# Performance work log

Measured on AMD Instinct MI355X. Metric: run time of the kernel, lower is better.

## Reference

```python
import jax, jax.numpy as jnp
import numpy as np

N_NODES = 100000
N_EDGES = 1600000
NUM_FEATURES = 128
HIDDEN = 64
NUM_CLASSES = 2


def _gcn_norm(edge_index, num_nodes):
    # PyG gcn_norm: add self-loops, symmetric degree normalization.
    loop = jnp.arange(num_nodes, dtype=edge_index.dtype)
    src = jnp.concatenate([edge_index[0], loop])
    dst = jnp.concatenate([edge_index[1], loop])
    deg = jax.ops.segment_sum(jnp.ones_like(src, dtype=jnp.float32), dst,
                              num_segments=num_nodes)
    dinv = jnp.where(deg > 0, jax.lax.rsqrt(deg), 0.0)
    norm = dinv[src] * dinv[dst]  # [E + N]
    return src, dst, norm


def _gcn_conv(x, src, dst, norm, W, b, num_nodes):
    h = x @ W  # linear transform first (PyG GCNConv)
    msg = h[src] * norm[:, None]  # gather + edge scaling, [E+N, H]
    out = jax.ops.segment_sum(msg, dst, num_segments=num_nodes)  # scatter-add
    return out + b


def setup_inputs() -> dict:
    key = jax.random.key(0)
    ks = jax.random.split(key, 8)
    x = jax.random.normal(ks[0], (N_NODES, NUM_FEATURES), dtype=jnp.float32)
    edge_index = jax.random.randint(ks[1], (2, N_EDGES), 0, N_NODES, dtype=jnp.int32)
    def glorot(k, shape):
        lim = np.sqrt(6.0 / (shape[0] + shape[1]))
        return jax.random.uniform(k, shape, jnp.float32, -lim, lim)
    return {
        "x": x,
        "edge_index": edge_index,
        "W1": glorot(ks[2], (NUM_FEATURES, HIDDEN)),
        "b1": jnp.zeros((HIDDEN,), jnp.float32),
        "W2": glorot(ks[3], (HIDDEN, HIDDEN)),
        "b2": jnp.zeros((HIDDEN,), jnp.float32),
        "W3": glorot(ks[4], (HIDDEN, HIDDEN)),
        "b3": jnp.zeros((HIDDEN,), jnp.float32),
        "Wlin": glorot(ks[5], (HIDDEN, NUM_CLASSES)),
        "blin": jnp.zeros((NUM_CLASSES,), jnp.float32),
    }


def reference(x, edge_index, W1, b1, W2, b2, W3, b3, Wlin, blin):
    num_nodes = x.shape[0]
    src, dst, norm = _gcn_norm(edge_index, num_nodes)
    # eval mode: dropout is identity
    h = jax.nn.relu(_gcn_conv(x, src, dst, norm, W1, b1, num_nodes))
    h = jax.nn.relu(_gcn_conv(h, src, dst, norm, W2, b2, num_nodes))
    h = jax.nn.relu(_gcn_conv(h, src, dst, norm, W3, b3, num_nodes))
    logits = h @ Wlin + blin
    return jax.nn.log_softmax(logits, axis=1)
```

## Files before the change

kernel.cpp:

```cpp
#include <hip/hip_runtime.h>
#include <cstdint>
#include <cstddef>

#define NF 128
#define NH 64


__global__ __launch_bounds__(256) void zero_kernel(int* __restrict__ p, int n) {
  int i = blockIdx.x * 256 + threadIdx.x;
  if (i < n) p[i] = 0;
}

__global__ __launch_bounds__(256) void count_kernel(const int* __restrict__ ei, int E,
                                                    int* __restrict__ cnt) {
  int e = blockIdx.x * 256 + threadIdx.x;
  if (e < E) atomicAdd(&cnt[ei[E + e]], 1);
}

__global__ __launch_bounds__(256) void partial_kernel(const int* __restrict__ cnt, int N,
                                                      int* __restrict__ part) {
  __shared__ int sd[256];
  int t = threadIdx.x;
  int idx = blockIdx.x * 1024 + t * 4;
  int s = 0;
#pragma unroll
  for (int j = 0; j < 4; ++j)
    if (idx + j < N) s += cnt[idx + j];
  sd[t] = s;
  __syncthreads();
  for (int off = 128; off > 0; off >>= 1) {
    if (t < off) sd[t] += sd[t + off];
    __syncthreads();
  }
  if (t == 0) part[blockIdx.x] = sd[0];
}

__global__ __launch_bounds__(128) void scanp_kernel(int* __restrict__ part, int NB,
                                                    int* __restrict__ rowptrN) {
  __shared__ int s[128];
  int t = threadIdx.x;
  int v = (t < NB) ? part[t] : 0;
  s[t] = v;
  __syncthreads();
  for (int off = 1; off < 128; off <<= 1) {
    int add = (t >= off) ? s[t - off] : 0;
    __syncthreads();
    s[t] += add;
    __syncthreads();
  }
  if (t < NB) part[t] = s[t] - v;
  if (t == 0) rowptrN[0] = s[127];
}

__global__ __launch_bounds__(256) void rowptr_kernel(const int* __restrict__ cnt,
                                                     const int* __restrict__ part,
                                                     int* __restrict__ rowptr,
                                                     float* __restrict__ dinv, int N) {
  __shared__ int s[256];
  int t = threadIdx.x;
  int idx = blockIdx.x * 1024 + t * 4;
  int c[4];
  int ts = 0;
#pragma unroll
  for (int j = 0; j < 4; ++j) {
    c[j] = (idx + j < N) ? cnt[idx + j] : 0;
    ts += c[j];
  }
  s[t] = ts;
  __syncthreads();
  for (int off = 1; off < 256; off <<= 1) {
    int add = (t >= off) ? s[t - off] : 0;
    __syncthreads();
    s[t] += add;
    __syncthreads();
  }
  int run = s[t] - ts + part[blockIdx.x];
#pragma unroll
  for (int j = 0; j < 4; ++j) {
    if (idx + j < N) {
      rowptr[idx + j] = run;
      dinv[idx + j] = rsqrtf((float)(c[j] + 1));
    }
    run += c[j];
  }
}

__global__ __launch_bounds__(256) void fill_kernel(const int* __restrict__ ei, int E,
                                                   const int* __restrict__ rowptr,
                                                   int* __restrict__ cnt2,
                                                   int* __restrict__ col) {
  int e = blockIdx.x * 256 + threadIdx.x;
  if (e >= E) return;
  int s = ei[e];
  int d = ei[E + e];
  int pos = rowptr[d] + atomicAdd(&cnt2[d], 1);
  col[pos] = s;
}


template <int K>
__global__ __launch_bounds__(256, 4) void gemm_kernel(const float* __restrict__ X,
                                                      const float* __restrict__ W,
                                                      float* __restrict__ H, int N) {
  __shared__ float XsT[64][68];
  __shared__ float Ws[64 * 64];
  const int tid = threadIdx.x;
  const int n0 = blockIdx.x * 64;
  const int tn = (tid >> 4) * 4;
  const int tf = (tid & 15) * 4;

  float acc[4][4];
#pragma unroll
  for (int i = 0; i < 4; ++i)
#pragma unroll
    for (int j = 0; j < 4; ++j) acc[i][j] = 0.f;

  for (int kt = 0; kt < K / 64; ++kt) {
    {
      const float4* Wg = (const float4*)(W + (size_t)kt * 64 * 64);
      float4* Wl = (float4*)Ws;
#pragma unroll
      for (int j = 0; j < 4; ++j) Wl[tid + j * 256] = Wg[tid + j * 256];
    }
#pragma unroll
    for (int j = 0; j < 4; ++j) {
      int idx = tid + j * 256;
      int n = idx >> 4;
      int kq = idx & 15;
      float4 v = make_float4(0.f, 0.f, 0.f, 0.f);
      if (n0 + n < N)
        v = *(const float4*)(X + (size_t)(n0 + n) * K + kt * 64 + kq * 4);
      XsT[kq * 4 + 0][n] = v.x;
      XsT[kq * 4 + 1][n] = v.y;
      XsT[kq * 4 + 2][n] = v.z;
      XsT[kq * 4 + 3][n] = v.w;
    }
    __syncthreads();
#pragma unroll 8
    for (int k = 0; k < 64; ++k) {
      float4 xv = *(const float4*)(&XsT[k][tn]);
      float4 wv = *(const float4*)(&Ws[k * 64 + tf]);
      acc[0][0] = fmaf(xv.x, wv.x, acc[0][0]);
      acc[0][1] = fmaf(xv.x, wv.y, acc[0][1]);
      acc[0][2] = fmaf(xv.x, wv.z, acc[0][2]);
      acc[0][3] = fmaf(xv.x, wv.w, acc[0][3]);
      acc[1][0] = fmaf(xv.y, wv.x, acc[1][0]);
      acc[1][1] = fmaf(xv.y, wv.y, acc[1][1]);
      acc[1][2] = fmaf(xv.y, wv.z, acc[1][2]);
      acc[1][3] = fmaf(xv.y, wv.w, acc[1][3]);
      acc[2][0] = fmaf(xv.z, wv.x, acc[2][0]);
      acc[2][1] = fmaf(xv.z, wv.y, acc[2][1]);
      acc[2][2] = fmaf(xv.z, wv.z, acc[2][2]);
      acc[2][3] = fmaf(xv.z, wv.w, acc[2][3]);
      acc[3][0] = fmaf(xv.w, wv.x, acc[3][0]);
      acc[3][1] = fmaf(xv.w, wv.y, acc[3][1]);
      acc[3][2] = fmaf(xv.w, wv.z, acc[3][2]);
      acc[3][3] = fmaf(xv.w, wv.w, acc[3][3]);
    }
    __syncthreads();
  }
#pragma unroll
  for (int i = 0; i < 4; ++i) {
    int n = n0 + tn + i;
    if (n < N)
      *(float4*)(H + (size_t)n * 64 + tf) =
          make_float4(acc[i][0], acc[i][1], acc[i][2], acc[i][3]);
  }
}

template <int FINAL>
__global__ __launch_bounds__(256) void prop_kernel(
    const float* __restrict__ H, const int* __restrict__ rowptr,
    const int* __restrict__ col, const float* __restrict__ dinv,
    const float* __restrict__ bias, const float* __restrict__ Wlin,
    const float* __restrict__ blin, float* __restrict__ out, int N) {
  int lane = threadIdx.x & 63;
  int n = blockIdx.x * 4 + (threadIdx.x >> 6);
  n = __builtin_amdgcn_readfirstlane(n);
  if (n >= N) return;
  int e0 = rowptr[n];
  int e1 = rowptr[n + 1];
  float di = dinv[n];
  float acc = H[(size_t)n * 64 + lane] * (di * di);
  int e = e0;
  for (; e + 4 <= e1; e += 4) {
    int s0 = col[e], s1 = col[e + 1], s2 = col[e + 2], s3 = col[e + 3];
    float w0 = dinv[s0] * di, w1 = dinv[s1] * di;
    float w2 = dinv[s2] * di, w3 = dinv[s3] * di;
    float h0 = H[(size_t)s0 * 64 + lane];
    float h1 = H[(size_t)s1 * 64 + lane];
    float h2 = H[(size_t)s2 * 64 + lane];
    float h3 = H[(size_t)s3 * 64 + lane];
    acc = fmaf(w0, h0, acc);
    acc = fmaf(w1, h1, acc);
    acc = fmaf(w2, h2, acc);
    acc = fmaf(w3, h3, acc);
  }
  for (; e < e1; ++e) {
    int s = col[e];
    acc = fmaf(dinv[s] * di, H[(size_t)s * 64 + lane], acc);
  }
  float r = acc + bias[lane];
  r = r > 0.f ? r : 0.f;
  if (FINAL == 0) {
    out[(size_t)n * 64 + lane] = r;
  } else {
    float t0 = r * Wlin[lane * 2 + 0];
    float t1 = r * Wlin[lane * 2 + 1];
#pragma unroll
    for (int off = 32; off > 0; off >>= 1) {
      t0 += __shfl_xor(t0, off, 64);
      t1 += __shfl_xor(t1, off, 64);
    }
    if (lane == 0) {
      float l0 = t0 + blin[0];
      float l1 = t1 + blin[1];
      float m = fmaxf(l0, l1);
      float lz = m + logf(expf(l0 - m) + expf(l1 - m));
      out[(size_t)n * 2 + 0] = l0 - lz;
      out[(size_t)n * 2 + 1] = l1 - lz;
    }
  }
}


extern "C" void kernel_launch(void* const* d_in, const int* in_sizes, int n_in,
                              void* d_out, int out_size, void* d_ws, size_t ws_size,
                              hipStream_t stream) {
  const float* x  = (const float*)d_in[0];
  const int*   ei = (const int*)d_in[1];
  const float* W1 = (const float*)d_in[2];
  const float* b1 = (const float*)d_in[3];
  const float* W2 = (const float*)d_in[4];
  const float* b2 = (const float*)d_in[5];
  const float* W3 = (const float*)d_in[6];
  const float* b3 = (const float*)d_in[7];
  const float* Wl = (const float*)d_in[8];
  const float* bl = (const float*)d_in[9];
  float* out = (float*)d_out;

  const int N = in_sizes[0] / NF;
  const int E = in_sizes[1] / 2;

  char* w = (char*)d_ws;
  size_t off = 0;
  auto alloc = [&](size_t bytes) {
    void* p = w + off;
    off += bytes;
    off = (off + 15) & ~(size_t)15;
    return p;
  };
  int*   cnt    = (int*)alloc((size_t)N * 4);
  int*   cnt2   = (int*)alloc((size_t)N * 4);
  int*   rowptr = (int*)alloc((size_t)(N + 1) * 4);
  int*   part   = (int*)alloc(256 * 4);
  float* dinv   = (float*)alloc((size_t)N * 4);
  int*   col    = (int*)alloc((size_t)E * 4);
  float* hA     = (float*)alloc((size_t)N * NH * 4);
  float* hB     = (float*)alloc((size_t)N * NH * 4);

  const int NB = (N + 1023) / 1024;

  hipLaunchKernelGGL(zero_kernel, dim3((2 * N + 255) / 256), dim3(256), 0, stream, cnt, 2 * N);
  hipLaunchKernelGGL(count_kernel, dim3((E + 255) / 256), dim3(256), 0, stream, ei, E, cnt);
  hipLaunchKernelGGL(partial_kernel, dim3(NB), dim3(256), 0, stream, cnt, N, part);
  hipLaunchKernelGGL(scanp_kernel, dim3(1), dim3(128), 0, stream, part, NB, rowptr + N);
  hipLaunchKernelGGL(rowptr_kernel, dim3(NB), dim3(256), 0, stream, cnt, part, rowptr, dinv, N);
  hipLaunchKernelGGL(fill_kernel, dim3((E + 255) / 256), dim3(256), 0, stream,
                     ei, E, rowptr, cnt2, col);

  hipLaunchKernelGGL(gemm_kernel<128>, dim3((N + 63) / 64), dim3(256), 0, stream, x, W1, hA, N);
  hipLaunchKernelGGL(prop_kernel<0>, dim3((N + 3) / 4), dim3(256), 0, stream,
                     hA, rowptr, col, dinv, b1, (const float*)nullptr,
                     (const float*)nullptr, hB, N);
  hipLaunchKernelGGL(gemm_kernel<64>, dim3((N + 63) / 64), dim3(256), 0, stream, hB, W2, hA, N);
  hipLaunchKernelGGL(prop_kernel<0>, dim3((N + 3) / 4), dim3(256), 0, stream,
                     hA, rowptr, col, dinv, b2, (const float*)nullptr,
                     (const float*)nullptr, hB, N);
  hipLaunchKernelGGL(gemm_kernel<64>, dim3((N + 63) / 64), dim3(256), 0, stream, hB, W3, hA, N);
  hipLaunchKernelGGL(prop_kernel<1>, dim3((N + 3) / 4), dim3(256), 0, stream,
                     hA, rowptr, col, dinv, b3, Wl, bl, out, N);
}
```

Measured before the change: 481.3 us.

## Fuse next-layer GEMM into propagation kernel and partition CSR fill by destination range

The propagation kernel now multiplies each aggregated row by the next layer's weight matrix, which it holds in registers after staging it through shared memory. This removes the separate 64x64 GEMM launches and the round trip of the hidden features through global memory. The kernel becomes persistent with a grid-stride loop over nodes and unrolls the neighbour gather by 8. The CSR fill is split into 8 passes over destination ranges to improve locality of the atomics and column writes, at the cost of rereading the edge list 8 times. Holding 64 weights per thread raises register pressure, and the shared-memory row exchange relies on a manual waitcnt with no barrier.

Result: slower. 558.1 us (+15.9%).

```diff
diff --git a/kernel.cpp b/kernel.cpp
--- a/kernel.cpp
+++ b/kernel.cpp
@@ -88,11 +88,13 @@
 __global__ __launch_bounds__(256) void fill_kernel(const int* __restrict__ ei, int E,
                                                    const int* __restrict__ rowptr,
                                                    int* __restrict__ cnt2,
-                                                   int* __restrict__ col) {
+                                                   int* __restrict__ col,
+                                                   int lo, int hi) {
   int e = blockIdx.x * 256 + threadIdx.x;
   if (e >= E) return;
+  int d = ei[E + e];
+  if (d < lo || d >= hi) return;
   int s = ei[e];
-  int d = ei[E + e];
   int pos = rowptr[d] + atomicAdd(&cnt2[d], 1);
   col[pos] = s;
 }
@@ -169,56 +171,86 @@
 }
 
 template <int FINAL>
-__global__ __launch_bounds__(256) void prop_kernel(
+__global__ __launch_bounds__(256, 4) void prop_fused_kernel(
     const float* __restrict__ H, const int* __restrict__ rowptr,
     const int* __restrict__ col, const float* __restrict__ dinv,
-    const float* __restrict__ bias, const float* __restrict__ Wlin,
+    const float* __restrict__ bias, const float* __restrict__ Wn,
     const float* __restrict__ blin, float* __restrict__ out, int N) {
-  int lane = threadIdx.x & 63;
-  int n = blockIdx.x * 4 + (threadIdx.x >> 6);
-  n = __builtin_amdgcn_readfirstlane(n);
-  if (n >= N) return;
-  int e0 = rowptr[n];
-  int e1 = rowptr[n + 1];
-  float di = dinv[n];
-  float acc = H[(size_t)n * 64 + lane] * (di * di);
-  int e = e0;
-  for (; e + 4 <= e1; e += 4) {
-    int s0 = col[e], s1 = col[e + 1], s2 = col[e + 2], s3 = col[e + 3];
-    float w0 = dinv[s0] * di, w1 = dinv[s1] * di;
-    float w2 = dinv[s2] * di, w3 = dinv[s3] * di;
-    float h0 = H[(size_t)s0 * 64 + lane];
-    float h1 = H[(size_t)s1 * 64 + lane];
-    float h2 = H[(size_t)s2 * 64 + lane];
-    float h3 = H[(size_t)s3 * 64 + lane];
-    acc = fmaf(w0, h0, acc);
-    acc = fmaf(w1, h1, acc);
-    acc = fmaf(w2, h2, acc);
-    acc = fmaf(w3, h3, acc);
-  }
-  for (; e < e1; ++e) {
-    int s = col[e];
-    acc = fmaf(dinv[s] * di, H[(size_t)s * 64 + lane], acc);
-  }
-  float r = acc + bias[lane];
-  r = r > 0.f ? r : 0.f;
-  if (FINAL == 0) {
-    out[(size_t)n * 64 + lane] = r;
-  } else {
-    float t0 = r * Wlin[lane * 2 + 0];
-    float t1 = r * Wlin[lane * 2 + 1];
-#pragma unroll
-    for (int off = 32; off > 0; off >>= 1) {
-      t0 += __shfl_xor(t0, off, 64);
-      t1 += __shfl_xor(t1, off, 64);
-    }
-    if (lane == 0) {
-      float l0 = t0 + blin[0];
-      float l1 = t1 + blin[1];
-      float m = fmaxf(l0, l1);
-      float lz = m + logf(expf(l0 - m) + expf(l1 - m));
-      out[(size_t)n * 2 + 0] = l0 - lz;
-      out[(size_t)n * 2 + 1] = l1 - lz;
+  __shared__ float Ws[64 * 64];
+  __shared__ float rbuf[4][64];
+  const int lane = threadIdx.x & 63;
+  const int widx = threadIdx.x >> 6;
+
+  float wcol[64];
+  if (!FINAL) {
+    for (int i = threadIdx.x; i < 64 * 64; i += 256) Ws[i] = Wn[i];
+    __syncthreads();
+#pragma unroll
+    for (int k = 0; k < 64; ++k) wcol[k] = Ws[k * 64 + lane];
+  }
+  float wl0 = 0.f, wl1 = 0.f, bl0 = 0.f, bl1 = 0.f;
+  if (FINAL) {
+    wl0 = Wn[lane * 2 + 0];
+    wl1 = Wn[lane * 2 + 1];
+    bl0 = blin[0];
+    bl1 = blin[1];
+  }
+  const float bv = bias[lane];
+
+  const int nwaves = gridDim.x * 4;
+  for (int n = blockIdx.x * 4 + widx; n < N; n += nwaves) {
+    int e0 = rowptr[n];
+    int e1 = rowptr[n + 1];
+    float di = dinv[n];
+    float acc = H[(size_t)n * 64 + lane] * (di * di);
+    int e = e0;
+    for (; e + 8 <= e1; e += 8) {
+      int s[8];
+      float wv[8], h[8];
+#pragma unroll
+      for (int j = 0; j < 8; ++j) s[j] = col[e + j];
+#pragma unroll
+      for (int j = 0; j < 8; ++j) wv[j] = dinv[s[j]] * di;
+#pragma unroll
+      for (int j = 0; j < 8; ++j) h[j] = H[(size_t)s[j] * 64 + lane];
+#pragma unroll
+      for (int j = 0; j < 8; ++j) acc = fmaf(wv[j], h[j], acc);
+    }
+    for (; e < e1; ++e) {
+      int s = col[e];
+      acc = fmaf(dinv[s] * di, H[(size_t)s * 64 + lane], acc);
+    }
+    float r = acc + bv;
+    r = r > 0.f ? r : 0.f;
+    if (FINAL) {
+      float t0 = r * wl0;
+      float t1 = r * wl1;
+#pragma unroll
+      for (int off = 32; off > 0; off >>= 1) {
+        t0 += __shfl_xor(t0, off, 64);
+        t1 += __shfl_xor(t1, off, 64);
+      }
+      if (lane == 0) {
+        float l0 = t0 + bl0;
+        float l1 = t1 + bl1;
+        float m = fmaxf(l0, l1);
+        float lz = m + logf(expf(l0 - m) + expf(l1 - m));
+        out[(size_t)n * 2 + 0] = l0 - lz;
+        out[(size_t)n * 2 + 1] = l1 - lz;
+      }
+    } else {
+      rbuf[widx][lane] = r;
+      asm volatile("s_waitcnt lgkmcnt(0)" ::: "memory");
+      float o = 0.f;
+#pragma unroll
+      for (int q = 0; q < 16; ++q) {
+        float4 rv = *(const float4*)(&rbuf[widx][q * 4]);
+        o = fmaf(rv.x, wcol[4 * q + 0], o);
+        o = fmaf(rv.y, wcol[4 * q + 1], o);
+        o = fmaf(rv.z, wcol[4 * q + 2], o);
+        o = fmaf(rv.w, wcol[4 * q + 3], o);
+      }
+      out[(size_t)n * 64 + lane] = o;
     }
   }
 }
@@ -266,18 +298,19 @@
   hipLaunchKernelGGL(partial_kernel, dim3(NB), dim3(256), 0, stream, cnt, N, part);
   hipLaunchKernelGGL(scanp_kernel, dim3(1), dim3(128), 0, stream, part, NB, rowptr + N);
   hipLaunchKernelGGL(rowptr_kernel, dim3(NB), dim3(256), 0, stream, cnt, part, rowptr, dinv, N);
-  hipLaunchKernelGGL(fill_kernel, dim3((E + 255) / 256), dim3(256), 0, stream,
-                     ei, E, rowptr, cnt2, col);
+
+  const int P = 8;
+  const int RW = (N + P - 1) / P;
+  for (int p = 0; p < P; ++p) {
+    hipLaunchKernelGGL(fill_kernel, dim3((E + 255) / 256), dim3(256), 0, stream,
+                       ei, E, rowptr, cnt2, col, p * RW, (p + 1) * RW);
+  }
 
   hipLaunchKernelGGL(gemm_kernel<128>, dim3((N + 63) / 64), dim3(256), 0, stream, x, W1, hA, N);
-  hipLaunchKernelGGL(prop_kernel<0>, dim3((N + 3) / 4), dim3(256), 0, stream,
-                     hA, rowptr, col, dinv, b1, (const float*)nullptr,
-                     (const float*)nullptr, hB, N);
-  hipLaunchKernelGGL(gemm_kernel<64>, dim3((N + 63) / 64), dim3(256), 0, stream, hB, W2, hA, N);
-  hipLaunchKernelGGL(prop_kernel<0>, dim3((N + 3) / 4), dim3(256), 0, stream,
-                     hA, rowptr, col, dinv, b2, (const float*)nullptr,
-                     (const float*)nullptr, hB, N);
-  hipLaunchKernelGGL(gemm_kernel<64>, dim3((N + 63) / 64), dim3(256), 0, stream, hB, W3, hA, N);
-  hipLaunchKernelGGL(prop_kernel<1>, dim3((N + 3) / 4), dim3(256), 0, stream,
+  hipLaunchKernelGGL(prop_fused_kernel<0>, dim3(2048), dim3(256), 0, stream,
+                     hA, rowptr, col, dinv, b1, W2, (const float*)nullptr, hB, N);
+  hipLaunchKernelGGL(prop_fused_kernel<0>, dim3(2048), dim3(256), 0, stream,
+                     hB, rowptr, col, dinv, b2, W3, (const float*)nullptr, hA, N);
+  hipLaunchKernelGGL(prop_fused_kernel<1>, dim3(2048), dim3(256), 0, stream,
                      hA, rowptr, col, dinv, b3, Wl, bl, out, N);
 }
```
